# Kernel tuning notes

Hardware: AMD Instinct MI355X
Metric: run time of the kernel (lower is better)

The kernel has to match this reference:

```python
import jax, jax.numpy as jnp
import numpy as np

HID = 2048 * 3  # infl_ratio = 3
EPS = 1e-5
P_DROP = 0.5


def sign_ste(x):
    # straight-through binarization: sign in fwd, identity in bwd
    return x + jax.lax.stop_gradient(jnp.sign(x) - x)


def batchnorm(x, g, b):
    # training-mode BatchNorm1d: batch stats, biased variance
    m = jnp.mean(x, axis=0)
    v = jnp.mean((x - m) ** 2, axis=0)
    return g * (x - m) / jnp.sqrt(v + EPS) + b


def hardtanh(x):
    return jnp.clip(x, -1.0, 1.0)


def dropout(x, u):
    # u ~ U[0,1); keep where u >= p, scale by 1/(1-p)
    return jnp.where(u >= P_DROP, x / (1.0 - P_DROP), 0.0)


def setup_inputs() -> dict:
    key = jax.random.key(0)
    ks = jax.random.split(key, 16)
    B = 512
    d = {}
    d['x'] = jax.random.normal(ks[0], (B, 784), dtype=jnp.float32)
    d['drop_mask_bin'] = jax.random.uniform(ks[1], (B, HID), dtype=jnp.float32)
    d['drop_mask_real'] = jax.random.uniform(ks[2], (B, HID), dtype=jnp.float32)
    s1 = 1.0 / np.sqrt(784)
    sh = 1.0 / np.sqrt(HID)
    d['w1'] = jax.random.uniform(ks[3], (HID, 784), jnp.float32, -s1, s1)
    d['b1'] = jax.random.uniform(ks[4], (HID,), jnp.float32, -s1, s1)
    d['w2'] = jax.random.uniform(ks[5], (HID, HID), jnp.float32, -sh, sh)
    d['b2'] = jax.random.uniform(ks[6], (HID,), jnp.float32, -sh, sh)
    d['w3'] = jax.random.uniform(ks[7], (HID, HID), jnp.float32, -sh, sh)
    d['b3'] = jax.random.uniform(ks[8], (HID,), jnp.float32, -sh, sh)
    d['w4'] = jax.random.uniform(ks[9], (10, HID), jnp.float32, -sh, sh)
    d['b4'] = jax.random.uniform(ks[10], (10,), jnp.float32, -sh, sh)
    for i, k in zip((1, 2, 3), (ks[11], ks[12], ks[13])):
        d[f'g{i}'] = jnp.ones((HID,), jnp.float32)
        d[f'be{i}'] = jnp.zeros((HID,), jnp.float32)
    return d


def reference(x, drop_mask_bin, drop_mask_real, w1, b1, w2, b2, w3, b3, w4, b4,
              g1, be1, g2, be2, g3, be3):
    sg = jax.lax.stop_gradient
    # layer 1: input dim 784 -> input NOT binarized; weights binarized
    Bout1 = x @ sign_ste(w1).T + b1
    Rout1 = sg(x @ w1.T + b1)
    Bout1 = hardtanh(batchnorm(Bout1, g1, be1))
    Rout1 = sg(hardtanh(batchnorm(Rout1, g1, be1)))
    # layer 2: binarize activations and weights on binary path
    Bout2 = sign_ste(Bout1) @ sign_ste(w2).T + b2
    Rout2 = sg(Rout1 @ w2.T + b2)
    Bout2 = hardtanh(batchnorm(Bout2, g2, be2))
    Rout2 = sg(hardtanh(batchnorm(Rout2, g2, be2)))
    # layer 3 + dropout
    Bout3 = sign_ste(Bout2) @ sign_ste(w3).T + b3
    Rout3 = sg(Rout2 @ w3.T + b3)
    Bout3 = hardtanh(batchnorm(dropout(Bout3, drop_mask_bin), g3, be3))
    Rout3 = sg(hardtanh(batchnorm(dropout(Rout3, drop_mask_real), g3, be3)))
    # classifier (real-valued Linear)
    out = Bout3 @ w4.T + b4
    logp = jax.nn.log_softmax(out, axis=1)
    return (logp, out, Bout1, Rout1, Bout2, Rout2, Bout3, Rout3)
```

## Files before the change

### kernel.cpp

```cpp
#include <hip/hip_runtime.h>


typedef _Float16 f16x8 __attribute__((ext_vector_type(8)));
typedef _Float16 f16x4 __attribute__((ext_vector_type(4)));
typedef float f32x4 __attribute__((ext_vector_type(4)));
typedef int i32x4 __attribute__((ext_vector_type(4)));

#define MFMA16(a, b, c) __builtin_amdgcn_mfma_f32_16x16x32_f16((a), (b), (c), 0, 0, 0)
#define MFMAI8K64(a, b, c) __builtin_amdgcn_mfma_i32_16x16x64_i8((a), (b), (c), 0, 0, 0)

#define HIDC 6144
#define BATCH 512

#define OFF_XH    0ull
#define OFF_Z1LO  851968ull
#define OFF_SB8   13434880ull
#define OFF_RF    16580608ull
#define OFF_STATS 22872064ull
#define OFF_PPART 23068672ull
#define OFF_ZPB   24641536ull
#define OFF_ZPR   37224448ull
#define OFF_ZPR2  49807360ull
#define OFF_ZPR3  62390272ull
#define OFF_W1V   74973184ull
#define OFF_WV    85196800ull
#define OFF_WS8   160694272ull
#define WS_NEED   198443008ull

#define A8_STRIDE 458752ull

__device__ __forceinline__ void load_lds16(const void* g, char* lds) {
  __builtin_amdgcn_global_load_lds((const __attribute__((address_space(1))) void*)g,
                                   (__attribute__((address_space(3))) void*)lds, 16, 0, 0);
}

__global__ __launch_bounds__(256) void k_prep_xq(const float* __restrict__ x,
                                                 char* __restrict__ a8,
                                                 _Float16* __restrict__ xh) {
  int idx = blockIdx.x * 256 + threadIdx.x;
  if (idx >= 512 * 896) return;
  int row = idx / 896, k = idx - row * 896;
  float v = (k < 784) ? x[(size_t)row * 784 + k] : 0.f;
  int q = (int)lrintf(v * 16777216.0f);
  int d0 = ((q + 128) & 255) - 128; q = (q - d0) >> 8;
  int d1 = ((q + 128) & 255) - 128; q = (q - d1) >> 8;
  int d2 = ((q + 128) & 255) - 128; q = (q - d2) >> 8;
  a8[idx] = (char)d0;
  a8[A8_STRIDE + idx] = (char)d1;
  a8[2 * A8_STRIDE + idx] = (char)d2;
  a8[3 * A8_STRIDE + idx] = (char)q;
  if (k < 832) xh[(size_t)row * 832 + k] = (_Float16)v;
}

__global__ __launch_bounds__(256) void k_prep_w1(const float* __restrict__ w,
                                                 char* __restrict__ s1,
                                                 _Float16* __restrict__ w1v) {
  int idx = blockIdx.x * 256 + threadIdx.x;
  if (idx >= 6144 * 896) return;
  int r = idx / 896, k = idx - r * 896;
  float v = (k < 784) ? w[(size_t)r * 784 + k] : 0.f;
  s1[idx] = v > 0.f ? 1 : (v < 0.f ? -1 : 0);
  if (k < 832) w1v[(size_t)r * 832 + k] = (_Float16)v;
}

__global__ __launch_bounds__(256) void k_conv_w23(const float* __restrict__ w,
                                                  _Float16* __restrict__ wv,
                                                  char* __restrict__ ws8) {
  int idx = blockIdx.x * 256 + threadIdx.x;
  size_t o8 = (size_t)idx * 8;
  const float* s = w + o8;
  float4 v0 = *(const float4*)s;
  float4 v1 = *(const float4*)(s + 4);
  float a[8] = {v0.x, v0.y, v0.z, v0.w, v1.x, v1.y, v1.z, v1.w};
  f16x8 hv;
  unsigned long long sbits = 0;
#pragma unroll
  for (int e = 0; e < 8; ++e) {
    hv[e] = (_Float16)a[e];
    char sg = a[e] > 0.f ? 1 : (a[e] < 0.f ? -1 : 0);
    sbits |= ((unsigned long long)(unsigned char)sg) << (8 * e);
  }
  *(f16x8*)(wv + o8) = hv;
  *(unsigned long long*)(ws8 + o8) = sbits;
}

struct MixJob {
  const void* A;
  const void* B;
  float* C;
  int K;
  int kstart;
  int ksteps;
  int is8;
};
struct Mix6 { MixJob j[6]; };

__global__ __launch_bounds__(256) void k_gemm_mix(Mix6 P) {
  __shared__ __align__(16) char smem[32768];
  MixJob J = P.j[0];
  if (blockIdx.z == 1) J = P.j[1];
  if (blockIdx.z == 2) J = P.j[2];
  if (blockIdx.z == 3) J = P.j[3];
  if (blockIdx.z == 4) J = P.j[4];
  if (blockIdx.z == 5) J = P.j[5];
  const int t = threadIdx.x;
  const int lane = t & 63, wid = t >> 6;
  const int wm = wid >> 1, wn = wid & 1;
  const int bn = blockIdx.x, bm = blockIdx.y;
  const size_t K = (size_t)J.K;

  if (J.is8) {
    const char* A = (const char*)J.A;
    const char* B = (const char*)J.B;
    i32x4 acc[4][4];
#pragma unroll
    for (int mf = 0; mf < 4; ++mf)
#pragma unroll
      for (int nf = 0; nf < 4; ++nf) acc[mf][nf] = (i32x4){0, 0, 0, 0};

    for (int kt = 0; kt < J.ksteps; ++kt) {
      const int k0 = J.kstart + kt * 128;
#pragma unroll
      for (int i = 0; i < 4; ++i) {
        int p = i * 256 + t;
        int r = p >> 3, c16 = p & 7;
        load_lds16(A + (size_t)(bm * 128 + r) * K + k0 + c16 * 16, smem + p * 16);
      }
#pragma unroll
      for (int i = 0; i < 4; ++i) {
        int p = i * 256 + t;
        int r = p >> 3, c16 = p & 7;
        load_lds16(B + (size_t)(bn * 128 + r) * K + k0 + c16 * 16, smem + 16384 + p * 16);
      }
      __syncthreads();
#pragma unroll
      for (int kk = 0; kk < 2; ++kk) {
        i32x4 av[4], bv[4];
#pragma unroll
        for (int mf = 0; mf < 4; ++mf) {
          int r = wm * 64 + mf * 16 + (lane & 15);
          av[mf] = *(const i32x4*)(smem + r * 128 + kk * 64 + (lane >> 4) * 16);
        }
#pragma unroll
        for (int nf = 0; nf < 4; ++nf) {
          int r = wn * 64 + nf * 16 + (lane & 15);
          bv[nf] = *(const i32x4*)(smem + 16384 + r * 128 + kk * 64 + (lane >> 4) * 16);
        }
#pragma unroll
        for (int mf = 0; mf < 4; ++mf)
#pragma unroll
          for (int nf = 0; nf < 4; ++nf) acc[mf][nf] = MFMAI8K64(av[mf], bv[nf], acc[mf][nf]);
      }
      __syncthreads();
    }
#pragma unroll
    for (int mf = 0; mf < 4; ++mf)
#pragma unroll
      for (int nf = 0; nf < 4; ++nf) {
        int col = bn * 128 + wn * 64 + nf * 16 + (lane & 15);
        int row0 = bm * 128 + wm * 64 + mf * 16 + ((lane >> 4) << 2);
#pragma unroll
        for (int rr = 0; rr < 4; ++rr) {
          J.C[(size_t)(row0 + rr) * HIDC + col] = (float)acc[mf][nf][rr];
        }
      }
  } else {
    const _Float16* A = (const _Float16*)J.A;
    const _Float16* B = (const _Float16*)J.B;
    f32x4 acc[4][4];
#pragma unroll
    for (int mf = 0; mf < 4; ++mf)
#pragma unroll
      for (int nf = 0; nf < 4; ++nf) acc[mf][nf] = (f32x4){0.f, 0.f, 0.f, 0.f};

    for (int kt = 0; kt < J.ksteps; ++kt) {
      const int k0 = J.kstart + kt * 64;
#pragma unroll
      for (int i = 0; i < 4; ++i) {
        int p = i * 256 + t;
        int r = p >> 3, c16 = p & 7;
        load_lds16(A + (size_t)(bm * 128 + r) * K + k0 + c16 * 8, smem + p * 16);
      }
#pragma unroll
      for (int i = 0; i < 4; ++i) {
        int p = i * 256 + t;
        int r = p >> 3, c16 = p & 7;
        load_lds16(B + (size_t)(bn * 128 + r) * K + k0 + c16 * 8, smem + 16384 + p * 16);
      }
      __syncthreads();
#pragma unroll
      for (int kk = 0; kk < 2; ++kk) {
        f16x8 av[4], bv[4];
#pragma unroll
        for (int mf = 0; mf < 4; ++mf) {
          int r = wm * 64 + mf * 16 + (lane & 15);
          av[mf] = *(const f16x8*)(smem + r * 128 + kk * 64 + (lane >> 4) * 16);
        }
#pragma unroll
        for (int nf = 0; nf < 4; ++nf) {
          int r = wn * 64 + nf * 16 + (lane & 15);
          bv[nf] = *(const f16x8*)(smem + 16384 + r * 128 + kk * 64 + (lane >> 4) * 16);
        }
#pragma unroll
        for (int mf = 0; mf < 4; ++mf)
#pragma unroll
          for (int nf = 0; nf < 4; ++nf) acc[mf][nf] = MFMA16(av[mf], bv[nf], acc[mf][nf]);
      }
      __syncthreads();
    }
#pragma unroll
    for (int mf = 0; mf < 4; ++mf)
#pragma unroll
      for (int nf = 0; nf < 4; ++nf) {
        int col = bn * 128 + wn * 64 + nf * 16 + (lane & 15);
        int row0 = bm * 128 + wm * 64 + mf * 16 + ((lane >> 4) << 2);
#pragma unroll
        for (int rr = 0; rr < 4; ++rr) {
          J.C[(size_t)(row0 + rr) * HIDC + col] = acc[mf][nf][rr];
        }
      }
  }
}

__global__ __launch_bounds__(256) void k_combine1(const float* __restrict__ D0,
                                                  const float* __restrict__ D1,
                                                  const float* __restrict__ D2,
                                                  const float* __restrict__ D3,
                                                  float* __restrict__ Zhi,
                                                  float* __restrict__ Zlo) {
  size_t i4 = ((size_t)blockIdx.x * 256 + threadIdx.x) * 4;
  float4 v0 = *(const float4*)(D0 + i4);
  float4 v1 = *(const float4*)(D1 + i4);
  float4 v2 = *(const float4*)(D2 + i4);
  float4 v3 = *(const float4*)(D3 + i4);
  const float* p0 = &v0.x;
  const float* p1 = &v1.x;
  const float* p2 = &v2.x;
  const float* p3 = &v3.x;
  float4 hi, lo;
  float* hp = &hi.x;
  float* lp = &lo.x;
#pragma unroll
  for (int e = 0; e < 4; ++e) {
    double zv = (((double)p3[e] * 256.0 + (double)p2[e]) * 256.0 + (double)p1[e]) * 256.0 +
                (double)p0[e];
    zv *= (1.0 / 16777216.0);
    float h = (float)zv;
    hp[e] = h;
    lp[e] = (float)(zv - (double)h);
  }
  *(float4*)(Zhi + i4) = hi;
  *(float4*)(Zlo + i4) = lo;
}

struct StJob { const float* Z; const float* Zp0; const float* Zp1; const float* Zp2;
               const float* msk; };
struct St2 { StJob j[2]; const float* bias; int dodrop; double* ppart; };

__global__ __launch_bounds__(256) void k_stats_part(St2 P) {
  __shared__ double sm[4][64];
  __shared__ double sq[4][64];
  const int z = blockIdx.z;
  StJob J = z ? P.j[1] : P.j[0];
  const int li = threadIdx.x & 63, rg = threadIdx.x >> 6;
  const int col = blockIdx.x * 64 + li;
  const double bb = P.dodrop ? (double)P.bias[col] : 0.0;
  double s = 0.0, s2 = 0.0;
#pragma unroll 4
  for (int rr = 0; rr < 16; ++rr) {
    int r = blockIdx.y * 64 + rg * 16 + rr;
    size_t i = (size_t)r * HIDC + col;
    double v = (double)J.Z[i];
    if (J.Zp0) v += (double)J.Zp0[i];
    if (J.Zp1) v += (double)J.Zp1[i];
    if (J.Zp2) v += (double)J.Zp2[i];
    if (P.dodrop) v = (J.msk[i] >= 0.5f) ? 2.0 * (v + bb) : 0.0;
    s += v;
    s2 += v * v;
  }
  sm[rg][li] = s;
  sq[rg][li] = s2;
  __syncthreads();
  if (rg == 0) {
    double S = sm[0][li] + sm[1][li] + sm[2][li] + sm[3][li];
    double S2 = sq[0][li] + sq[1][li] + sq[2][li] + sq[3][li];
    size_t o = ((size_t)(z * 8 + blockIdx.y) * 2) * HIDC + col;
    P.ppart[o] = S;
    P.ppart[o + HIDC] = S2;
  }
}

__global__ __launch_bounds__(256) void k_stats_fin(const double* __restrict__ ppart,
                                                   double* __restrict__ stats) {
  const int z = blockIdx.z;
  const int c = blockIdx.x * 256 + threadIdx.x;
  double S = 0.0, S2 = 0.0;
#pragma unroll
  for (int y = 0; y < 8; ++y) {
    size_t o = ((size_t)(z * 8 + y) * 2) * HIDC + c;
    S += ppart[o];
    S2 += ppart[o + HIDC];
  }
  double m = S / 512.0;
  double var = S2 / 512.0 - m * m;
  stats[z * 2 * HIDC + c] = m;
  stats[z * 2 * HIDC + HIDC + c] = 1.0 / sqrt(var + 1e-5);
}

struct BnJob { float* Z; const float* Zp0; const float* Zp1; const float* Zp2;
               void* aux; const float* msk; int auxmode; };
struct Bn2 {
  BnJob j[2];
  const double* stats;
  const float* g; const float* be; const float* bias;
  int dodrop;
};

__global__ __launch_bounds__(256) void k_bn2(Bn2 P) {
  const int z = blockIdx.z;
  BnJob J = z ? P.j[1] : P.j[0];
  const double* m_arr = P.stats + (size_t)z * 2 * HIDC;
  const double* r_arr = m_arr + HIDC;
  int idx = blockIdx.x * 256 + threadIdx.x;
  int row = idx / 1536;
  int c4 = (idx - row * 1536) * 4;
  size_t base = (size_t)row * HIDC + c4;
  float4 zv = *(const float4*)(J.Z + base);
  float zz[4] = {zv.x, zv.y, zv.z, zv.w};
  double ex[4] = {0.0, 0.0, 0.0, 0.0};
  if (J.Zp0) {
    float4 t4 = *(const float4*)(J.Zp0 + base);
    ex[0] += t4.x; ex[1] += t4.y; ex[2] += t4.z; ex[3] += t4.w;
  }
  if (J.Zp1) {
    float4 t4 = *(const float4*)(J.Zp1 + base);
    ex[0] += t4.x; ex[1] += t4.y; ex[2] += t4.z; ex[3] += t4.w;
  }
  if (J.Zp2) {
    float4 t4 = *(const float4*)(J.Zp2 + base);
    ex[0] += t4.x; ex[1] += t4.y; ex[2] += t4.z; ex[3] += t4.w;
  }
  float mk[4] = {1.f, 1.f, 1.f, 1.f};
  if (P.dodrop) {
    float4 t4 = *(const float4*)(J.msk + base);
    mk[0] = t4.x; mk[1] = t4.y; mk[2] = t4.z; mk[3] = t4.w;
  }
  float o[4];
  f16x4 a4;
  int sbits = 0;
#pragma unroll
  for (int e = 0; e < 4; ++e) {
    int c = c4 + e;
    double v = (double)zz[e] + ex[e];
    if (P.dodrop) v = (mk[e] >= 0.5f) ? 2.0 * (v + (double)P.bias[c]) : 0.0;
    double bnv = (double)P.g[c] * ((v - m_arr[c]) * r_arr[c]) + (double)P.be[c];
    bnv = bnv > 1.0 ? 1.0 : (bnv < -1.0 ? -1.0 : bnv);
    o[e] = (float)bnv;
    char sg = bnv > 0.0 ? 1 : (bnv < 0.0 ? -1 : 0);
    sbits |= ((int)(unsigned char)sg) << (8 * e);
    a4[e] = (_Float16)o[e];
  }
  float4 ov = {o[0], o[1], o[2], o[3]};
  *(float4*)(J.Z + base) = ov;
  if (J.auxmode == 0) *(int*)((char*)J.aux + base) = sbits;
  if (J.auxmode == 1) *(f16x4*)((_Float16*)J.aux + base) = a4;
}

__global__ __launch_bounds__(256) void k_head(const float* __restrict__ B3,
                                              const float* __restrict__ w4,
                                              const float* __restrict__ b4,
                                              float* __restrict__ out,
                                              float* __restrict__ logp) {
  const int row = blockIdx.x, t = threadIdx.x;
  float acc[10];
#pragma unroll
  for (int j = 0; j < 10; ++j) acc[j] = 0.f;
  const float* a = B3 + (size_t)row * HIDC;
  for (int k4 = t; k4 < 1536; k4 += 256) {
    float4 av = *(const float4*)(a + k4 * 4);
#pragma unroll
    for (int j = 0; j < 10; ++j) {
      float4 wv = *(const float4*)(w4 + (size_t)j * HIDC + k4 * 4);
      acc[j] += av.x * wv.x + av.y * wv.y + av.z * wv.z + av.w * wv.w;
    }
  }
#pragma unroll
  for (int j = 0; j < 10; ++j)
    for (int off = 32; off; off >>= 1) acc[j] += __shfl_down(acc[j], off);
  __shared__ float sred[4][10];
  int wid = t >> 6, ln = t & 63;
  if (ln == 0)
#pragma unroll
    for (int j = 0; j < 10; ++j) sred[wid][j] = acc[j];
  __syncthreads();
  if (t == 0) {
    double o[10];
    double mx = -1e300;
#pragma unroll
    for (int j = 0; j < 10; ++j) {
      o[j] = (double)sred[0][j] + sred[1][j] + sred[2][j] + sred[3][j] + (double)b4[j];
      mx = o[j] > mx ? o[j] : mx;
    }
    double s = 0.0;
#pragma unroll
    for (int j = 0; j < 10; ++j) s += exp(o[j] - mx);
    double l = log(s) + mx;
#pragma unroll
    for (int j = 0; j < 10; ++j) {
      out[row * 10 + j] = (float)o[j];
      logp[row * 10 + j] = (float)(o[j] - l);
    }
  }
}

extern "C" void kernel_launch(void* const* d_in, const int* in_sizes, int n_in,
                              void* d_out, int out_size, void* d_ws, size_t ws_size,
                              hipStream_t stream) {
  const float* x   = (const float*)d_in[0];
  const float* mkb = (const float*)d_in[1];
  const float* mkr = (const float*)d_in[2];
  const float* w1  = (const float*)d_in[3];
  const float* w2  = (const float*)d_in[5];
  const float* w3  = (const float*)d_in[7];
  const float* b3  = (const float*)d_in[8];
  const float* w4  = (const float*)d_in[9];
  const float* b4  = (const float*)d_in[10];
  const float* g1  = (const float*)d_in[11]; const float* be1 = (const float*)d_in[12];
  const float* g2  = (const float*)d_in[13]; const float* be2 = (const float*)d_in[14];
  const float* g3  = (const float*)d_in[15]; const float* be3 = (const float*)d_in[16];

  float* outp = (float*)d_out;
  float* logp = outp;
  float* outo = outp + 5120;
  float* B1 = outp + 10240;
  float* R1 = outp + 3155968;
  float* B2 = outp + 6301696;
  float* R2 = outp + 9447424;
  float* B3 = outp + 12593152;
  float* R3 = outp + 15738880;

  char* ws = (char*)d_ws;
  _Float16* xh  = (_Float16*)(ws + OFF_XH);
  float* z1lo   = (float*)(ws + OFF_Z1LO);
  char* sB8     = (char*)(ws + OFF_SB8);
  _Float16* rF  = (_Float16*)(ws + OFF_RF);
  double* stats = (double*)(ws + OFF_STATS);
  double* ppart = (double*)(ws + OFF_PPART);
  float* zpb    = (float*)(ws + OFF_ZPB);
  float* zpr    = (float*)(ws + OFF_ZPR);
  float* zpr2   = (float*)(ws + OFF_ZPR2);
  float* zpr3   = (float*)(ws + OFF_ZPR3);
  _Float16* w1v = (_Float16*)(ws + OFF_W1V);
  _Float16* wv  = (_Float16*)(ws + OFF_WV);
  char* ws8     = (char*)(ws + OFF_WS8);
  char* a8 = (char*)(ws + OFF_WS8);
  char* s1 = (char*)(ws + OFF_WS8 + 4ull * A8_STRIDE);

  k_prep_xq<<<1792, 256, 0, stream>>>(x, a8, xh);
  k_prep_w1<<<21504, 256, 0, stream>>>(w1, s1, w1v);
  {
    Mix6 P{};
    P.j[0] = {a8,                 s1, zpb,  896, 0, 7, 1};
    P.j[1] = {a8 + A8_STRIDE,     s1, zpr,  896, 0, 7, 1};
    P.j[2] = {a8 + 2 * A8_STRIDE, s1, zpr2, 896, 0, 7, 1};
    P.j[3] = {a8 + 3 * A8_STRIDE, s1, zpr3, 896, 0, 7, 1};
    P.j[4] = {xh, w1v, R1, 832, 0, 13, 0};
    P.j[5] = P.j[4];
    k_gemm_mix<<<dim3(48, 4, 5), 256, 0, stream>>>(P);
  }
  k_combine1<<<3072, 256, 0, stream>>>(zpb, zpr, zpr2, zpr3, B1, z1lo);
  {
    St2 S{};
    S.j[0] = {B1, z1lo, nullptr, nullptr, nullptr};
    S.j[1] = {R1, nullptr, nullptr, nullptr, nullptr};
    S.bias = nullptr; S.dodrop = 0; S.ppart = ppart;
    k_stats_part<<<dim3(96, 8, 2), 256, 0, stream>>>(S);
    k_stats_fin<<<dim3(24, 1, 2), 256, 0, stream>>>(ppart, stats);
    Bn2 B{};
    B.j[0] = {B1, z1lo, nullptr, nullptr, sB8, nullptr, 0};
    B.j[1] = {R1, nullptr, nullptr, nullptr, rF, nullptr, 1};
    B.stats = stats; B.g = g1; B.be = be1; B.bias = nullptr; B.dodrop = 0;
    k_bn2<<<dim3(3072, 1, 2), 256, 0, stream>>>(B);
  }
  k_conv_w23<<<18432, 256, 0, stream>>>(w2, wv, ws8);
  {
    Mix6 P{};
    P.j[0] = {sB8, ws8, B2,   HIDC, 0,    24, 1};
    P.j[1] = {sB8, ws8, zpb,  HIDC, 3072, 24, 1};
    P.j[2] = {rF,  wv,  R2,   HIDC, 0,    24, 0};
    P.j[3] = {rF,  wv,  zpr,  HIDC, 1536, 24, 0};
    P.j[4] = {rF,  wv,  zpr2, HIDC, 3072, 24, 0};
    P.j[5] = {rF,  wv,  zpr3, HIDC, 4608, 24, 0};
    k_gemm_mix<<<dim3(48, 4, 6), 256, 0, stream>>>(P);
  }
  {
    St2 S{};
    S.j[0] = {B2, zpb, nullptr, nullptr, nullptr};
    S.j[1] = {R2, zpr, zpr2, zpr3, nullptr};
    S.bias = nullptr; S.dodrop = 0; S.ppart = ppart;
    k_stats_part<<<dim3(96, 8, 2), 256, 0, stream>>>(S);
    k_stats_fin<<<dim3(24, 1, 2), 256, 0, stream>>>(ppart, stats);
    Bn2 B{};
    B.j[0] = {B2, zpb, nullptr, nullptr, sB8, nullptr, 0};
    B.j[1] = {R2, zpr, zpr2, zpr3, rF, nullptr, 1};
    B.stats = stats; B.g = g2; B.be = be2; B.bias = nullptr; B.dodrop = 0;
    k_bn2<<<dim3(3072, 1, 2), 256, 0, stream>>>(B);
  }
  k_conv_w23<<<18432, 256, 0, stream>>>(w3, wv, ws8);
  {
    Mix6 P{};
    P.j[0] = {sB8, ws8, B3,   HIDC, 0,    24, 1};
    P.j[1] = {sB8, ws8, zpb,  HIDC, 3072, 24, 1};
    P.j[2] = {rF,  wv,  R3,   HIDC, 0,    24, 0};
    P.j[3] = {rF,  wv,  zpr,  HIDC, 1536, 24, 0};
    P.j[4] = {rF,  wv,  zpr2, HIDC, 3072, 24, 0};
    P.j[5] = {rF,  wv,  zpr3, HIDC, 4608, 24, 0};
    k_gemm_mix<<<dim3(48, 4, 6), 256, 0, stream>>>(P);
  }
  {
    St2 S{};
    S.j[0] = {B3, zpb, nullptr, nullptr, mkb};
    S.j[1] = {R3, zpr, zpr2, zpr3, mkr};
    S.bias = b3; S.dodrop = 1; S.ppart = ppart;
    k_stats_part<<<dim3(96, 8, 2), 256, 0, stream>>>(S);
    k_stats_fin<<<dim3(24, 1, 2), 256, 0, stream>>>(ppart, stats);
    Bn2 B{};
    B.j[0] = {B3, zpb, nullptr, nullptr, nullptr, mkb, 2};
    B.j[1] = {R3, zpr, zpr2, zpr3, nullptr, mkr, 2};
    B.stats = stats; B.g = g3; B.be = be3; B.bias = b3; B.dodrop = 1;
    k_bn2<<<dim3(3072, 1, 2), 256, 0, stream>>>(B);
  }
  k_head<<<512, 256, 0, stream>>>(B3, w4, b4, outo, logp);
}
```

Baseline: 559.7 us.

## Double-buffer LDS tiles in mixed int8/fp16 GEMM to overlap loads with MFMA

Doubles shared memory to two 32KB stages and issues global-to-LDS loads for the next K tile before computing on the current one. Uses explicit s_waitcnt vmcnt(8) so only the previous stage's loads must land, then raw s_barrier. This is meant to hide global memory latency behind MFMA work. In exchange, 64KB of LDS per block lowers occupancy, and correctness now depends on the hand-counted vmcnt matching the eight outstanding loads.

```diff
diff --git a/kernel.cpp b/kernel.cpp
--- a/kernel.cpp
+++ b/kernel.cpp
@@ -96,7 +96,7 @@
 struct Mix6 { MixJob j[6]; };
 
 __global__ __launch_bounds__(256) void k_gemm_mix(Mix6 P) {
-  __shared__ __align__(16) char smem[32768];
+  __shared__ __align__(16) char smem[65536];
   MixJob J = P.j[0];
   if (blockIdx.z == 1) J = P.j[1];
   if (blockIdx.z == 2) J = P.j[2];
@@ -108,6 +108,7 @@
   const int wm = wid >> 1, wn = wid & 1;
   const int bn = blockIdx.x, bm = blockIdx.y;
   const size_t K = (size_t)J.K;
+  const int nt = J.ksteps;
 
   if (J.is8) {
     const char* A = (const char*)J.A;
@@ -118,40 +119,51 @@
 #pragma unroll
       for (int nf = 0; nf < 4; ++nf) acc[mf][nf] = (i32x4){0, 0, 0, 0};
 
-    for (int kt = 0; kt < J.ksteps; ++kt) {
-      const int k0 = J.kstart + kt * 128;
+    auto stage = [&](char* dst, int k0) {
 #pragma unroll
       for (int i = 0; i < 4; ++i) {
         int p = i * 256 + t;
         int r = p >> 3, c16 = p & 7;
-        load_lds16(A + (size_t)(bm * 128 + r) * K + k0 + c16 * 16, smem + p * 16);
+        load_lds16(A + (size_t)(bm * 128 + r) * K + k0 + c16 * 16, dst + p * 16);
       }
 #pragma unroll
       for (int i = 0; i < 4; ++i) {
         int p = i * 256 + t;
         int r = p >> 3, c16 = p & 7;
-        load_lds16(B + (size_t)(bn * 128 + r) * K + k0 + c16 * 16, smem + 16384 + p * 16);
-      }
-      __syncthreads();
+        load_lds16(B + (size_t)(bn * 128 + r) * K + k0 + c16 * 16, dst + 16384 + p * 16);
+      }
+    };
+
+    stage(smem, J.kstart);
+    for (int kt = 0; kt < nt; ++kt) {
+      char* cbuf = smem + (kt & 1) * 32768;
+      char* nbuf = smem + ((kt + 1) & 1) * 32768;
+      if (kt + 1 < nt) {
+        stage(nbuf, J.kstart + (kt + 1) * 128);
+        asm volatile("s_waitcnt vmcnt(8)" ::: "memory");
+      } else {
+        asm volatile("s_waitcnt vmcnt(0)" ::: "memory");
+      }
+      __builtin_amdgcn_s_barrier();
 #pragma unroll
       for (int kk = 0; kk < 2; ++kk) {
         i32x4 av[4], bv[4];
 #pragma unroll
         for (int mf = 0; mf < 4; ++mf) {
           int r = wm * 64 + mf * 16 + (lane & 15);
-          av[mf] = *(const i32x4*)(smem + r * 128 + kk * 64 + (lane >> 4) * 16);
+          av[mf] = *(const i32x4*)(cbuf + r * 128 + kk * 64 + (lane >> 4) * 16);
         }
 #pragma unroll
         for (int nf = 0; nf < 4; ++nf) {
           int r = wn * 64 + nf * 16 + (lane & 15);
-          bv[nf] = *(const i32x4*)(smem + 16384 + r * 128 + kk * 64 + (lane >> 4) * 16);
+          bv[nf] = *(const i32x4*)(cbuf + 16384 + r * 128 + kk * 64 + (lane >> 4) * 16);
         }
 #pragma unroll
         for (int mf = 0; mf < 4; ++mf)
 #pragma unroll
           for (int nf = 0; nf < 4; ++nf) acc[mf][nf] = MFMAI8K64(av[mf], bv[nf], acc[mf][nf]);
       }
-      __syncthreads();
+      __builtin_amdgcn_s_barrier();
     }
 #pragma unroll
     for (int mf = 0; mf < 4; ++mf)
@@ -173,40 +185,51 @@
 #pragma unroll
       for (int nf = 0; nf < 4; ++nf) acc[mf][nf] = (f32x4){0.f, 0.f, 0.f, 0.f};
 
-    for (int kt = 0; kt < J.ksteps; ++kt) {
-      const int k0 = J.kstart + kt * 64;
+    auto stage = [&](char* dst, int k0) {
 #pragma unroll
       for (int i = 0; i < 4; ++i) {
         int p = i * 256 + t;
         int r = p >> 3, c16 = p & 7;
-        load_lds16(A + (size_t)(bm * 128 + r) * K + k0 + c16 * 8, smem + p * 16);
+        load_lds16(A + (size_t)(bm * 128 + r) * K + k0 + c16 * 8, dst + p * 16);
       }
 #pragma unroll
       for (int i = 0; i < 4; ++i) {
         int p = i * 256 + t;
         int r = p >> 3, c16 = p & 7;
-        load_lds16(B + (size_t)(bn * 128 + r) * K + k0 + c16 * 8, smem + 16384 + p * 16);
-      }
-      __syncthreads();
+        load_lds16(B + (size_t)(bn * 128 + r) * K + k0 + c16 * 8, dst + 16384 + p * 16);
+      }
+    };
+
+    stage(smem, J.kstart);
+    for (int kt = 0; kt < nt; ++kt) {
+      char* cbuf = smem + (kt & 1) * 32768;
+      char* nbuf = smem + ((kt + 1) & 1) * 32768;
+      if (kt + 1 < nt) {
+        stage(nbuf, J.kstart + (kt + 1) * 64);
+        asm volatile("s_waitcnt vmcnt(8)" ::: "memory");
+      } else {
+        asm volatile("s_waitcnt vmcnt(0)" ::: "memory");
+      }
+      __builtin_amdgcn_s_barrier();
 #pragma unroll
       for (int kk = 0; kk < 2; ++kk) {
         f16x8 av[4], bv[4];
 #pragma unroll
         for (int mf = 0; mf < 4; ++mf) {
           int r = wm * 64 + mf * 16 + (lane & 15);
-          av[mf] = *(const f16x8*)(smem + r * 128 + kk * 64 + (lane >> 4) * 16);
+          av[mf] = *(const f16x8*)(cbuf + r * 128 + kk * 64 + (lane >> 4) * 16);
         }
 #pragma unroll
         for (int nf = 0; nf < 4; ++nf) {
           int r = wn * 64 + nf * 16 + (lane & 15);
-          bv[nf] = *(const f16x8*)(smem + 16384 + r * 128 + kk * 64 + (lane >> 4) * 16);
+          bv[nf] = *(const f16x8*)(cbuf + 16384 + r * 128 + kk * 64 + (lane >> 4) * 16);
         }
 #pragma unroll
         for (int mf = 0; mf < 4; ++mf)
 #pragma unroll
           for (int nf = 0; nf < 4; ++nf) acc[mf][nf] = MFMA16(av[mf], bv[nf], acc[mf][nf]);
       }
-      __syncthreads();
+      __builtin_amdgcn_s_barrier();
     }
 #pragma unroll
     for (int mf = 0; mf < 4; ++mf)
```

Measured after the change: 500.4 us. 10.6% less time.
